# Performance work log

Hardware: AMD Instinct MI355X
Metric: run time of the kernel (lower is better)

The kernel has to match this reference:

```python
import jax, jax.numpy as jnp
import numpy as np

LEAK = 0.01  # torch LeakyReLU default negative_slope

def lrelu(x):
    return jnp.where(x >= 0, x, LEAK * x)

def edge_conv(x, src, dst, ea, W1, b1, W2, b2):
    # message: cat(x_i=target, x_j=source, edge_attr) -> Linear -> LeakyReLU -> Linear
    m = jnp.concatenate([x[dst], x[src], ea], axis=1)          # [E, 2F+Fe]
    h = lrelu(m @ W1 + b1) @ W2 + b2                            # [E, H]
    n = x.shape[0]
    agg = jnp.full((n, h.shape[1]), jnp.inf, h.dtype).at[dst].min(h)  # scatter-min at target
    return jnp.where(jnp.isfinite(agg), agg, jnp.zeros_like(agg))     # empty nodes -> 0


def setup_inputs() -> dict:
    key = jax.random.key(0)
    ks = jax.random.split(key, 20)
    B, N, E = 4, 20000, 640000
    NF, AD, EF, H = 2, 1, 1, 8
    inp = {
        "node_features": jax.random.randint(ks[0], (B, N, NF), 0, 10, dtype=jnp.int32),
        "actions": jax.random.normal(ks[1], (B, N), dtype=jnp.float32),
        "edge_index": jax.random.randint(ks[2], (B, 2, E), 0, N, dtype=jnp.int64),
        "edge_features": jax.random.normal(ks[3], (B, E, EF), dtype=jnp.float32),
    }
    d0 = NF + AD  # 3
    def lin(k, fin, fout):
        s = 1.0 / np.sqrt(fin)
        k1, k2 = jax.random.split(k)
        return (jax.random.uniform(k1, (fin, fout), jnp.float32, -s, s),
                jax.random.uniform(k2, (fout,), jnp.float32, -s, s))
    inp["c1_W1"], inp["c1_b1"] = lin(ks[4], 2 * d0 + EF, H)
    inp["c1_W2"], inp["c1_b2"] = lin(ks[5], H, H)
    inp["c2_W1"], inp["c2_b1"] = lin(ks[6], 2 * H + 1, H)
    inp["c2_W2"], inp["c2_b2"] = lin(ks[7], H, H)
    inp["c3_W1"], inp["c3_b1"] = lin(ks[8], 2 * H + 1, H)
    inp["c3_W2"], inp["c3_b2"] = lin(ks[9], H, H)
    inp["lin_W"], inp["lin_b"] = lin(ks[10], d0 + H, 1)
    return inp


def reference(node_features, actions, edge_index, edge_features,
              c1_W1, c1_b1, c1_W2, c1_b2,
              c2_W1, c2_b1, c2_W2, c2_b2,
              c3_W1, c3_b1, c3_W2, c3_b2,
              lin_W, lin_b):
    # x = int(node_features) concat actions  -> float
    x0 = jnp.concatenate([node_features.astype(jnp.int32).astype(jnp.float32),
                          actions[..., None]], axis=-1)  # [B,N,3]

    def per_graph(x0g, eig, eag):
        src, dst = eig[0], eig[1]  # flow source_to_target: x_j=src, x_i=dst
        h = lrelu(edge_conv(x0g, src, dst, eag, c1_W1, c1_b1, c1_W2, c1_b2))
        h = lrelu(edge_conv(h, src, dst, eag, c2_W1, c2_b1, c2_W2, c2_b2))
        h = lrelu(edge_conv(h, src, dst, eag, c3_W1, c3_b1, c3_W2, c3_b2))
        xc = jnp.concatenate([x0g, h], axis=1)  # [N, 3+8]
        return jnp.sum(xc, axis=0)              # sum-pool over nodes

    pooled = jax.vmap(per_graph)(x0, edge_index, edge_features)  # [B, 11]
    return pooled @ lin_W + lin_b  # [B, 1]
```

## Files before the change

kernel.cpp:

```cpp
#include <hip/hip_runtime.h>

#define LEAK 0.01f
#define BS 128
#define PCHUNK 4096
#define PT 512
#define CT 512
#define MAXNB 256
#define CPGMAX 256

__device__ __forceinline__ float lrelu(float v) {
    return v >= 0.f ? v : LEAK * v;
}

__device__ __forceinline__ unsigned int fmin_encode(float x) {
    unsigned int u = __float_as_uint(x);
    return (u & 0x80000000u) ? ~u : (u | 0x80000000u);
}
__device__ __forceinline__ float fmin_decode(unsigned int k) {
    unsigned int u = (k & 0x80000000u) ? (k ^ 0x80000000u) : ~k;
    return __uint_as_float(u);
}

__device__ __forceinline__ unsigned int bf16_rne(float f) {
    unsigned int u = __float_as_uint(f);
    return (u + 0x7FFFu + ((u >> 16) & 1u)) >> 16;
}

__device__ __forceinline__ void block_add(float c, float* dst) {
    __shared__ float wsum[8];
#pragma unroll
    for (int off = 32; off > 0; off >>= 1) c += __shfl_down(c, off, 64);
    int lane = threadIdx.x & 63;
    int wave = threadIdx.x >> 6;
    if (lane == 0) wsum[wave] = c;
    __syncthreads();
    if (threadIdx.x == 0) {
        float s = 0.f;
        int nw = blockDim.x >> 6;
        for (int w = 0; w < nw; ++w) s += wsum[w];
        atomicAdd(dst, s);
    }
}

__global__ __launch_bounds__(PT) void part_init_kernel(
    const int* __restrict__ ei, const float* __restrict__ ea,
    int2* __restrict__ pairs, int* __restrict__ ofs,
    const int* __restrict__ nf, const float* __restrict__ act,
    const float* __restrict__ W1, const float* __restrict__ b1,
    const float* __restrict__ lw, const float* __restrict__ lb,
    float* __restrict__ a1, unsigned short* __restrict__ a2,
    float* __restrict__ out, int E, int N, int NB, int CPG) {
    int b = blockIdx.y;
    int t = threadIdx.x;

    if (blockIdx.x >= CPG) {
        int n = (blockIdx.x - CPG) * PT + t;
        float c = 0.f;
        if (n < N) {
            size_t i = (size_t)b * N + n;
            float x0 = (float)nf[i * 2 + 0];
            float x1 = (float)nf[i * 2 + 1];
            float x2 = act[i];
            float v1[8], v2[8];
#pragma unroll
            for (int j = 0; j < 8; ++j) {
                v1[j] = b1[j] + x0 * W1[0 * 8 + j] + x1 * W1[1 * 8 + j] + x2 * W1[2 * 8 + j];
                v2[j] =         x0 * W1[3 * 8 + j] + x1 * W1[4 * 8 + j] + x2 * W1[5 * 8 + j];
            }
            float4* o1 = (float4*)(a1 + i * 8);
            o1[0] = make_float4(v1[0], v1[1], v1[2], v1[3]);
            o1[1] = make_float4(v1[4], v1[5], v1[6], v1[7]);
            unsigned int w[4];
#pragma unroll
            for (int q = 0; q < 4; ++q)
                w[q] = bf16_rne(v2[2 * q]) | (bf16_rne(v2[2 * q + 1]) << 16);
            *(int4*)(a2 + i * 8) = make_int4(w[0], w[1], w[2], w[3]);
            c = x0 * lw[0] + x1 * lw[1] + x2 * lw[2];
            if (n == 0) c += lb[0];
        }
        block_add(c, &out[b]);
        return;
    }

    __shared__ int lc[MAXNB];
    __shared__ int lofs[MAXNB + 1];
    __shared__ int ts[PT];
    int c = blockIdx.x;
    for (int i = t; i < NB; i += PT) lc[i] = 0;
    __syncthreads();

    int e0 = c * PCHUNK;
    int end = min(e0 + PCHUNK, E);
    const int* srow = ei + (size_t)b * 2 * E;
    const int* drow = srow + E;

    int pk[PCHUNK / PT];
#pragma unroll
    for (int j = 0; j < PCHUNK / PT; ++j) {
        int e = e0 + j * PT + t;
        int p = -1;
        if (e < end) {
            int d = drow[e];
            int bin = d >> 7;
            int r = atomicAdd(&lc[bin], 1);
            p = bin | ((d & 127) << 10) | (r << 17);
        }
        pk[j] = p;
    }
    __syncthreads();

    int v = (t < NB) ? lc[t] : 0;
    ts[t] = v;
    __syncthreads();
    int incl = v;
    for (int off = 1; off < PT; off <<= 1) {
        int add = (t >= off) ? ts[t - off] : 0;
        __syncthreads();
        incl += add;
        ts[t] = incl;
        __syncthreads();
    }
    if (t < NB) lofs[t] = incl - v;
    if (t == PT - 1) lofs[NB] = incl;
    __syncthreads();

    for (int i = t; i <= NB; i += PT) {
        int w = lofs[i];
        ofs[((size_t)b * (NB + 1) + i) * CPG + c] = w;
        if (i < NB) lc[i] = w;
    }
    __syncthreads();

    size_t pbase = (size_t)b * E + e0;
#pragma unroll
    for (int j = 0; j < PCHUNK / PT; ++j) {
        int e = e0 + j * PT + t;
        if (e < end) {
            int p = pk[j];
            int bin = p & 1023;
            int dl = (p >> 10) & 127;
            int r = p >> 17;
            int pos = lc[bin] + r;
            pairs[pbase + pos] =
                make_int2(srow[e] | (dl << 16), __float_as_int(ea[(size_t)b * E + e]));
        }
    }
}


__device__ __forceinline__ void conv_edge_compute(
    const float* we, const float* bb, const float* __restrict__ W2,
    int2 p, int4 raw, const float* __restrict__ a1s,
    unsigned int* __restrict__ acc) {
    int dl = (p.x >> 16) & 127;
    float eav = __int_as_float(p.y);
    unsigned int wq[4] = {(unsigned int)raw.x, (unsigned int)raw.y,
                          (unsigned int)raw.z, (unsigned int)raw.w};
    float a2v[8];
#pragma unroll
    for (int q = 0; q < 4; ++q) {
        a2v[2 * q]     = __uint_as_float(wq[q] << 16);
        a2v[2 * q + 1] = __uint_as_float(wq[q] & 0xFFFF0000u);
    }
    float h1[8];
#pragma unroll
    for (int j = 0; j < 8; ++j) {
        h1[j] = a1s[dl * 9 + j] + a2v[j];
        h1[j] = fmaf(eav, we[j], h1[j]);
        h1[j] = lrelu(h1[j]);
    }
    float h2[8];
#pragma unroll
    for (int j = 0; j < 8; ++j) h2[j] = bb[j];
#pragma unroll
    for (int kk = 0; kk < 8; ++kk) {
        float hk = h1[kk];
#pragma unroll
        for (int j = 0; j < 8; ++j) h2[j] = fmaf(hk, W2[kk * 8 + j], h2[j]);
    }
#pragma unroll
    for (int j = 0; j < 8; ++j)
        atomicMin(&acc[dl * 9 + j], fmin_encode(h2[j]));
}

__device__ __forceinline__ void conv_edges_runs(
    const unsigned short* __restrict__ a2g, const float* we, const float* bb,
    const float* __restrict__ W2, const int2* __restrict__ pairsg,
    const int* __restrict__ ofb, int CPG,
    const float* __restrict__ a1s, unsigned int* __restrict__ acc,
    int* __restrict__ rs, int* __restrict__ re) {
    int t = threadIdx.x;
    for (int c = t; c < CPG; c += CT) {
        rs[c] = ofb[c];
        re[c] = ofb[CPG + c];
    }
    __syncthreads();
    int sw = t >> 5, sub = t & 31;
    const int nsw = CT >> 5;
    int c = sw;
    int2 pcur = make_int2(0, 0);
    int4 vcur = make_int4(0, 0, 0, 0);
    int kcur = 0, k1cur = 0;
    bool haveCur = false;
    if (c < CPG) {
        int cb = c * PCHUNK;
        kcur = cb + rs[c] + sub;
        k1cur = cb + re[c];
        if (kcur < k1cur) {
            pcur = pairsg[kcur];
            vcur = *(const int4*)(a2g + (size_t)(pcur.x & 0xFFFF) * 8);
            haveCur = true;
        }
    }
    while (c < CPG) {
        int cn = c + nsw;
        int2 pnext = make_int2(0, 0);
        int4 vnext = make_int4(0, 0, 0, 0);
        int knext = 0, k1next = 0;
        bool haveNext = false;
        if (cn < CPG) {
            int cb = cn * PCHUNK;
            knext = cb + rs[cn] + sub;
            k1next = cb + re[cn];
            if (knext < k1next) {
                pnext = pairsg[knext];
                vnext = *(const int4*)(a2g + (size_t)(pnext.x & 0xFFFF) * 8);
                haveNext = true;
            }
        }
        if (haveCur) {
            conv_edge_compute(we, bb, W2, pcur, vcur, a1s, acc);
            for (int k = kcur + 32; k < k1cur; k += 32) {
                int2 p = pairsg[k];
                int4 v = *(const int4*)(a2g + (size_t)(p.x & 0xFFFF) * 8);
                conv_edge_compute(we, bb, W2, p, v, a1s, acc);
            }
        }
        c = cn; pcur = pnext; vcur = vnext; kcur = knext; k1cur = k1next;
        haveCur = haveNext;
    }
}

__global__ __launch_bounds__(CT) void conv_mid_kernel(
    const float* __restrict__ a1, const unsigned short* __restrict__ a2,
    const float* __restrict__ w1e, const float* __restrict__ W2,
    const float* __restrict__ b2,
    const float* __restrict__ nW1, const float* __restrict__ nb1,
    const int* __restrict__ ofs, const int2* __restrict__ pairs,
    float* __restrict__ na1, unsigned short* __restrict__ na2,
    int N, int NB, int CPG, int E) {
    __shared__ float a1s[BS * 9];
    __shared__ unsigned int acc[BS * 9];
    __shared__ int rs[CPGMAX];
    __shared__ int re[CPGMAX];
    int b = blockIdx.y;
    int bin = blockIdx.x;
    int n0 = bin << 7;
    int nCnt = min(BS, N - n0);
    int t = threadIdx.x;
    size_t node0 = (size_t)b * N + n0;

    for (int i = t; i < nCnt * 8; i += CT)
        a1s[(i >> 3) * 9 + (i & 7)] = a1[node0 * 8 + i];
    for (int i = t; i < BS * 9; i += CT) acc[i] = 0xFFFFFFFFu;
    float we[8], bb[8];
#pragma unroll
    for (int j = 0; j < 8; ++j) { we[j] = w1e[j]; bb[j] = b2[j]; }
    __syncthreads();

    conv_edges_runs(a2 + (size_t)b * N * 8, we, bb, W2,
                    pairs + (size_t)b * E,
                    ofs + ((size_t)b * (NB + 1) + bin) * CPG,
                    CPG, a1s, acc, rs, re);
    __syncthreads();

    for (int i = t; i < nCnt * 8; i += CT) {
        float v = fmin_decode(acc[(i >> 3) * 9 + (i & 7)]);
        unsigned int u = __float_as_uint(v);
        if ((u & 0x7F800000u) == 0x7F800000u) v = 0.f;
        a1s[(i >> 3) * 9 + (i & 7)] = lrelu(v);
    }
    __syncthreads();

    for (int nh = t; nh < nCnt * 2; nh += CT) {
        int node = nh >> 1, half = nh & 1;
        float h[8];
#pragma unroll
        for (int j = 0; j < 8; ++j) h[j] = a1s[node * 9 + j];
        float v[8];
#pragma unroll
        for (int j = 0; j < 8; ++j) v[j] = half ? 0.f : nb1[j];
        const float* Wbase = nW1 + (half ? 64 : 0);
#pragma unroll
        for (int k = 0; k < 8; ++k) {
            float hk = h[k];
#pragma unroll
            for (int j = 0; j < 8; ++j) v[j] = fmaf(hk, Wbase[k * 8 + j], v[j]);
        }
        if (half) {
            unsigned int w[4];
#pragma unroll
            for (int q = 0; q < 4; ++q)
                w[q] = bf16_rne(v[2 * q]) | (bf16_rne(v[2 * q + 1]) << 16);
            *(int4*)(na2 + (node0 + node) * 8) = make_int4(w[0], w[1], w[2], w[3]);
        } else {
            float4* o = (float4*)(na1 + (node0 + node) * 8);
            o[0] = make_float4(v[0], v[1], v[2], v[3]);
            o[1] = make_float4(v[4], v[5], v[6], v[7]);
        }
    }
}

__global__ __launch_bounds__(CT) void conv_final_kernel(
    const float* __restrict__ a1, const unsigned short* __restrict__ a2,
    const float* __restrict__ w1e, const float* __restrict__ W2,
    const float* __restrict__ b2, const float* __restrict__ lw,
    const int* __restrict__ ofs, const int2* __restrict__ pairs,
    float* __restrict__ out, int N, int NB, int CPG, int E) {
    __shared__ float a1s[BS * 9];
    __shared__ unsigned int acc[BS * 9];
    __shared__ int rs[CPGMAX];
    __shared__ int re[CPGMAX];
    int b = blockIdx.y;
    int bin = blockIdx.x;
    int n0 = bin << 7;
    int nCnt = min(BS, N - n0);
    int t = threadIdx.x;
    size_t node0 = (size_t)b * N + n0;

    for (int i = t; i < nCnt * 8; i += CT)
        a1s[(i >> 3) * 9 + (i & 7)] = a1[node0 * 8 + i];
    for (int i = t; i < BS * 9; i += CT) acc[i] = 0xFFFFFFFFu;
    float we[8], bb[8];
#pragma unroll
    for (int j = 0; j < 8; ++j) { we[j] = w1e[j]; bb[j] = b2[j]; }
    __syncthreads();

    conv_edges_runs(a2 + (size_t)b * N * 8, we, bb, W2,
                    pairs + (size_t)b * E,
                    ofs + ((size_t)b * (NB + 1) + bin) * CPG,
                    CPG, a1s, acc, rs, re);
    __syncthreads();

    float c = 0.f;
    if (t < nCnt) {
#pragma unroll
        for (int j = 0; j < 8; ++j) {
            float v = fmin_decode(acc[t * 9 + j]);
            unsigned int u = __float_as_uint(v);
            if ((u & 0x7F800000u) == 0x7F800000u) v = 0.f;
            c = fmaf(lrelu(v), lw[3 + j], c);
        }
    }
    __syncthreads();
    block_add(c, &out[b]);
}


__global__ __launch_bounds__(256) void node_init_kernel(
    const int* __restrict__ nf, const float* __restrict__ act,
    float* __restrict__ x0, int BN) {
    int tid = blockIdx.x * blockDim.x + threadIdx.x;
    if (tid >= BN) return;
    x0[tid * 3 + 0] = (float)nf[tid * 2 + 0];
    x0[tid * 3 + 1] = (float)nf[tid * 2 + 1];
    x0[tid * 3 + 2] = act[tid];
}

template <int D>
__global__ __launch_bounds__(256) void edge_conv_kernel(
    const float* __restrict__ x, const int* __restrict__ ei,
    const float* __restrict__ ea,
    const float* __restrict__ W1, const float* __restrict__ b1,
    const float* __restrict__ W2, const float* __restrict__ b2,
    unsigned int* __restrict__ agg, int E, int N, int B) {
    int tid = blockIdx.x * blockDim.x + threadIdx.x;
    if (tid >= B * E) return;
    int b = tid / E;
    int e = tid - b * E;
    const int* eb = ei + (size_t)b * 2 * E;
    int s = eb[e];
    int d = eb[E + e];
    const float* xi = x + ((size_t)b * N + d) * D;
    const float* xj = x + ((size_t)b * N + s) * D;
    constexpr int M = 2 * D + 1;
    float m[M];
#pragma unroll
    for (int k = 0; k < D; ++k) { m[k] = xi[k]; m[D + k] = xj[k]; }
    m[2 * D] = ea[(size_t)b * E + e];
    float h1[8];
#pragma unroll
    for (int j = 0; j < 8; ++j) h1[j] = b1[j];
#pragma unroll
    for (int k = 0; k < M; ++k) {
        float mk = m[k];
#pragma unroll
        for (int j = 0; j < 8; ++j) h1[j] = fmaf(mk, W1[k * 8 + j], h1[j]);
    }
#pragma unroll
    for (int j = 0; j < 8; ++j) h1[j] = lrelu(h1[j]);
    float h2[8];
#pragma unroll
    for (int j = 0; j < 8; ++j) h2[j] = b2[j];
#pragma unroll
    for (int k = 0; k < 8; ++k) {
        float hk = h1[k];
#pragma unroll
        for (int j = 0; j < 8; ++j) h2[j] = fmaf(hk, W2[k * 8 + j], h2[j]);
    }
    unsigned int* ag = agg + ((size_t)b * N + d) * 8;
#pragma unroll
    for (int j = 0; j < 8; ++j) atomicMin(&ag[j], fmin_encode(h2[j]));
}

__global__ __launch_bounds__(256) void finalize_kernel(
    unsigned int* __restrict__ agg, int total) {
    int tid = blockIdx.x * blockDim.x + threadIdx.x;
    if (tid >= total) return;
    float v = fmin_decode(agg[tid]);
    unsigned int u = __float_as_uint(v);
    if ((u & 0x7F800000u) == 0x7F800000u) v = 0.f;
    ((float*)agg)[tid] = lrelu(v);
}

__global__ __launch_bounds__(256) void pool_kernel(
    const float* __restrict__ x0, const float* __restrict__ h,
    const float* __restrict__ lw, const float* __restrict__ lb,
    float* __restrict__ out, int N) {
    int b = blockIdx.y;
    int n = blockIdx.x * blockDim.x + threadIdx.x;
    float c = 0.f;
    if (n < N) {
        const float* x = x0 + ((size_t)b * N + n) * 3;
        const float* hh = h + ((size_t)b * N + n) * 8;
        c = x[0] * lw[0] + x[1] * lw[1] + x[2] * lw[2];
#pragma unroll
        for (int k = 0; k < 8; ++k) c = fmaf(hh[k], lw[3 + k], c);
        if (n == 0) c += lb[0];
    }
    block_add(c, &out[b]);
}


static inline size_t align256(size_t x) { return (x + 255) & ~(size_t)255; }

extern "C" void kernel_launch(void* const* d_in, const int* in_sizes, int n_in,
                              void* d_out, int out_size, void* d_ws, size_t ws_size,
                              hipStream_t stream) {
    const int B = 4;
    const int N = in_sizes[1] / B;
    const int E = in_sizes[2] / (2 * B);

    const int*   nf  = (const int*)d_in[0];
    const float* act = (const float*)d_in[1];
    const int*   ei  = (const int*)d_in[2];
    const float* ea  = (const float*)d_in[3];
    const float* c1_W1 = (const float*)d_in[4];
    const float* c1_b1 = (const float*)d_in[5];
    const float* c1_W2 = (const float*)d_in[6];
    const float* c1_b2 = (const float*)d_in[7];
    const float* c2_W1 = (const float*)d_in[8];
    const float* c2_b1 = (const float*)d_in[9];
    const float* c2_W2 = (const float*)d_in[10];
    const float* c2_b2 = (const float*)d_in[11];
    const float* c3_W1 = (const float*)d_in[12];
    const float* c3_b1 = (const float*)d_in[13];
    const float* c3_W2 = (const float*)d_in[14];
    const float* c3_b2 = (const float*)d_in[15];
    const float* lw    = (const float*)d_in[16];
    const float* lb    = (const float*)d_in[17];
    float* out = (float*)d_out;

    const int BN = B * N;
    const int BE = B * E;
    const int NB = (N + BS - 1) / BS;
    const int CPG = (E + PCHUNK - 1) / PCHUNK;

    char* ws = (char*)d_ws;
    size_t off = 0;
    float* a1A = (float*)(ws + off);           off += align256((size_t)BN * 8 * 4);
    float* a1B = (float*)(ws + off);           off += align256((size_t)BN * 8 * 4);
    unsigned short* a2A = (unsigned short*)(ws + off); off += align256((size_t)BN * 8 * 2);
    unsigned short* a2B = (unsigned short*)(ws + off); off += align256((size_t)BN * 8 * 2);
    int* ofs    = (int*)(ws + off);    off += align256((size_t)B * (NB + 1) * CPG * 4);
    int2* pairs = (int2*)(ws + off);   off += align256((size_t)BE * 8);
    float* x0   = (float*)(ws + off);  off += align256((size_t)BN * 3 * 4);
    const bool useFast = (off <= ws_size) && (NB <= MAXNB) && (CPG <= CPGMAX) &&
                         (N <= 32768);

    hipMemsetAsync(out, 0, (size_t)B * sizeof(float), stream);

    if (useFast) {
        const int initBlocks = (N + PT - 1) / PT;
        dim3 pgrid(CPG + initBlocks, B);
        dim3 cgrid(NB, B);

        part_init_kernel<<<pgrid, PT, 0, stream>>>(
            ei, ea, pairs, ofs, nf, act, c1_W1, c1_b1, lw, lb,
            a1A, a2A, out, E, N, NB, CPG);

        conv_mid_kernel<<<cgrid, CT, 0, stream>>>(
            a1A, a2A, c1_W1 + 6 * 8, c1_W2, c1_b2, c2_W1, c2_b1,
            ofs, pairs, a1B, a2B, N, NB, CPG, E);
        conv_mid_kernel<<<cgrid, CT, 0, stream>>>(
            a1B, a2B, c2_W1 + 16 * 8, c2_W2, c2_b2, c3_W1, c3_b1,
            ofs, pairs, a1A, a2A, N, NB, CPG, E);
        conv_final_kernel<<<cgrid, CT, 0, stream>>>(
            a1A, a2A, c3_W1 + 16 * 8, c3_W2, c3_b2, lw,
            ofs, pairs, out, N, NB, CPG, E);
    } else {
        const int egrid = (BE + 255) / 256;
        const int aggTotal = BN * 8;
        const int agrid = (aggTotal + 255) / 256;
        const size_t aggBytes = (size_t)aggTotal * 4;
        unsigned int* uA = (unsigned int*)a1A;
        unsigned int* uB = (unsigned int*)a1B;

        node_init_kernel<<<(BN + 255) / 256, 256, 0, stream>>>(nf, act, x0, BN);

        hipMemsetAsync(uA, 0xFF, aggBytes, stream);
        edge_conv_kernel<3><<<egrid, 256, 0, stream>>>(
            x0, ei, ea, c1_W1, c1_b1, c1_W2, c1_b2, uA, E, N, B);
        finalize_kernel<<<agrid, 256, 0, stream>>>(uA, aggTotal);

        hipMemsetAsync(uB, 0xFF, aggBytes, stream);
        edge_conv_kernel<8><<<egrid, 256, 0, stream>>>(
            (const float*)uA, ei, ea, c2_W1, c2_b1, c2_W2, c2_b2, uB, E, N, B);
        finalize_kernel<<<agrid, 256, 0, stream>>>(uB, aggTotal);

        hipMemsetAsync(uA, 0xFF, aggBytes, stream);
        edge_conv_kernel<8><<<egrid, 256, 0, stream>>>(
            (const float*)uB, ei, ea, c3_W1, c3_b1, c3_W2, c3_b2, uA, E, N, B);
        finalize_kernel<<<agrid, 256, 0, stream>>>(uA, aggTotal);

        dim3 plgrid((N + 255) / 256, B);
        pool_kernel<<<plgrid, 256, 0, stream>>>(x0, (const float*)uA, lw, lb, out, N);
    }
}
```

Measured before the change: 219.7 us.

## Fuse partition and three conv stages into one cooperative kernel with grid syncs

Merges the partition/init kernel and the three edge-conv stage kernels into a single cooperative mega-kernel that separates stages with grid.sync and threadfence. This removes three kernel launch boundaries and the associated drain and refill gaps. The launch is used only when occupancy allows the whole grid (max(CPG+initBlocks, NB) × B blocks) to be resident, and falls back to the separate kernels otherwise. It also drops the software prefetch of the next chunk in the edge loop, and the mega-kernel carries the union of shared memory with launch bounds of 8 blocks, which may change register allocation.

Result: faster. 208.7 us (median of 2 runs) (-5.0%).

```diff
diff --git a/kernel.cpp b/kernel.cpp
--- a/kernel.cpp
+++ b/kernel.cpp
@@ -1,4 +1,7 @@
 #include <hip/hip_runtime.h>
+#include <hip/hip_cooperative_groups.h>
+
+namespace cg = cooperative_groups;
 
 #define LEAK 0.01f
 #define BS 128
@@ -42,50 +45,47 @@
     }
 }
 
-__global__ __launch_bounds__(PT) void part_init_kernel(
-    const int* __restrict__ ei, const float* __restrict__ ea,
-    int2* __restrict__ pairs, int* __restrict__ ofs,
+
+__device__ void init_body(
     const int* __restrict__ nf, const float* __restrict__ act,
     const float* __restrict__ W1, const float* __restrict__ b1,
     const float* __restrict__ lw, const float* __restrict__ lb,
     float* __restrict__ a1, unsigned short* __restrict__ a2,
-    float* __restrict__ out, int E, int N, int NB, int CPG) {
-    int b = blockIdx.y;
+    float* __restrict__ out, int N, int b, int ib) {
     int t = threadIdx.x;
-
-    if (blockIdx.x >= CPG) {
-        int n = (blockIdx.x - CPG) * PT + t;
-        float c = 0.f;
-        if (n < N) {
-            size_t i = (size_t)b * N + n;
-            float x0 = (float)nf[i * 2 + 0];
-            float x1 = (float)nf[i * 2 + 1];
-            float x2 = act[i];
-            float v1[8], v2[8];
-#pragma unroll
-            for (int j = 0; j < 8; ++j) {
-                v1[j] = b1[j] + x0 * W1[0 * 8 + j] + x1 * W1[1 * 8 + j] + x2 * W1[2 * 8 + j];
-                v2[j] =         x0 * W1[3 * 8 + j] + x1 * W1[4 * 8 + j] + x2 * W1[5 * 8 + j];
-            }
-            float4* o1 = (float4*)(a1 + i * 8);
-            o1[0] = make_float4(v1[0], v1[1], v1[2], v1[3]);
-            o1[1] = make_float4(v1[4], v1[5], v1[6], v1[7]);
-            unsigned int w[4];
-#pragma unroll
-            for (int q = 0; q < 4; ++q)
-                w[q] = bf16_rne(v2[2 * q]) | (bf16_rne(v2[2 * q + 1]) << 16);
-            *(int4*)(a2 + i * 8) = make_int4(w[0], w[1], w[2], w[3]);
-            c = x0 * lw[0] + x1 * lw[1] + x2 * lw[2];
-            if (n == 0) c += lb[0];
-        }
-        block_add(c, &out[b]);
-        return;
-    }
-
-    __shared__ int lc[MAXNB];
-    __shared__ int lofs[MAXNB + 1];
-    __shared__ int ts[PT];
-    int c = blockIdx.x;
+    int n = ib * PT + t;
+    float c = 0.f;
+    if (n < N) {
+        size_t i = (size_t)b * N + n;
+        float x0 = (float)nf[i * 2 + 0];
+        float x1 = (float)nf[i * 2 + 1];
+        float x2 = act[i];
+        float v1[8], v2[8];
+#pragma unroll
+        for (int j = 0; j < 8; ++j) {
+            v1[j] = b1[j] + x0 * W1[0 * 8 + j] + x1 * W1[1 * 8 + j] + x2 * W1[2 * 8 + j];
+            v2[j] =         x0 * W1[3 * 8 + j] + x1 * W1[4 * 8 + j] + x2 * W1[5 * 8 + j];
+        }
+        float4* o1 = (float4*)(a1 + i * 8);
+        o1[0] = make_float4(v1[0], v1[1], v1[2], v1[3]);
+        o1[1] = make_float4(v1[4], v1[5], v1[6], v1[7]);
+        unsigned int w[4];
+#pragma unroll
+        for (int q = 0; q < 4; ++q)
+            w[q] = bf16_rne(v2[2 * q]) | (bf16_rne(v2[2 * q + 1]) << 16);
+        *(int4*)(a2 + i * 8) = make_int4(w[0], w[1], w[2], w[3]);
+        c = x0 * lw[0] + x1 * lw[1] + x2 * lw[2];
+        if (n == 0) c += lb[0];
+    }
+    block_add(c, &out[b]);
+}
+
+__device__ void part_body(
+    const int* __restrict__ ei, const float* __restrict__ ea,
+    int2* __restrict__ pairs, int* __restrict__ ofs,
+    int E, int NB, int CPG, int b, int c,
+    int* __restrict__ lc, int* __restrict__ lofs, int* __restrict__ ts) {
+    int t = threadIdx.x;
     for (int i = t; i < NB; i += PT) lc[i] = 0;
     __syncthreads();
 
@@ -147,7 +147,6 @@
     }
 }
 
-
 __device__ __forceinline__ void conv_edge_compute(
     const float* we, const float* bb, const float* __restrict__ W2,
     int2 p, int4 raw, const float* __restrict__ a1s,
@@ -183,7 +182,7 @@
         atomicMin(&acc[dl * 9 + j], fmin_encode(h2[j]));
 }
 
-__device__ __forceinline__ void conv_edges_runs(
+__device__ void conv_edges_runs(
     const unsigned short* __restrict__ a2g, const float* we, const float* bb,
     const float* __restrict__ W2, const int2* __restrict__ pairsg,
     const int* __restrict__ ofb, int CPG,
@@ -197,48 +196,193 @@
     __syncthreads();
     int sw = t >> 5, sub = t & 31;
     const int nsw = CT >> 5;
-    int c = sw;
-    int2 pcur = make_int2(0, 0);
-    int4 vcur = make_int4(0, 0, 0, 0);
-    int kcur = 0, k1cur = 0;
-    bool haveCur = false;
-    if (c < CPG) {
+    for (int c = sw; c < CPG; c += nsw) {
         int cb = c * PCHUNK;
-        kcur = cb + rs[c] + sub;
-        k1cur = cb + re[c];
-        if (kcur < k1cur) {
-            pcur = pairsg[kcur];
-            vcur = *(const int4*)(a2g + (size_t)(pcur.x & 0xFFFF) * 8);
-            haveCur = true;
-        }
-    }
-    while (c < CPG) {
-        int cn = c + nsw;
-        int2 pnext = make_int2(0, 0);
-        int4 vnext = make_int4(0, 0, 0, 0);
-        int knext = 0, k1next = 0;
-        bool haveNext = false;
-        if (cn < CPG) {
-            int cb = cn * PCHUNK;
-            knext = cb + rs[cn] + sub;
-            k1next = cb + re[cn];
-            if (knext < k1next) {
-                pnext = pairsg[knext];
-                vnext = *(const int4*)(a2g + (size_t)(pnext.x & 0xFFFF) * 8);
-                haveNext = true;
-            }
-        }
-        if (haveCur) {
-            conv_edge_compute(we, bb, W2, pcur, vcur, a1s, acc);
-            for (int k = kcur + 32; k < k1cur; k += 32) {
-                int2 p = pairsg[k];
-                int4 v = *(const int4*)(a2g + (size_t)(p.x & 0xFFFF) * 8);
-                conv_edge_compute(we, bb, W2, p, v, a1s, acc);
-            }
-        }
-        c = cn; pcur = pnext; vcur = vnext; kcur = knext; k1cur = k1next;
-        haveCur = haveNext;
-    }
+        int k1 = cb + re[c];
+        for (int k = cb + rs[c] + sub; k < k1; k += 32) {
+            int2 p = pairsg[k];
+            int4 v = *(const int4*)(a2g + (size_t)(p.x & 0xFFFF) * 8);
+            conv_edge_compute(we, bb, W2, p, v, a1s, acc);
+        }
+    }
+}
+
+__device__ void conv_mid_body(
+    const float* __restrict__ a1, const unsigned short* __restrict__ a2,
+    const float* __restrict__ w1e, const float* __restrict__ W2,
+    const float* __restrict__ b2,
+    const float* __restrict__ nW1, const float* __restrict__ nb1,
+    const int* __restrict__ ofs, const int2* __restrict__ pairs,
+    float* __restrict__ na1, unsigned short* __restrict__ na2,
+    int N, int NB, int CPG, int E, int b, int bin,
+    float* __restrict__ a1s, unsigned int* __restrict__ acc,
+    int* __restrict__ rs, int* __restrict__ re) {
+    int n0 = bin << 7;
+    int nCnt = min(BS, N - n0);
+    int t = threadIdx.x;
+    size_t node0 = (size_t)b * N + n0;
+
+    for (int i = t; i < nCnt * 8; i += CT)
+        a1s[(i >> 3) * 9 + (i & 7)] = a1[node0 * 8 + i];
+    for (int i = t; i < BS * 9; i += CT) acc[i] = 0xFFFFFFFFu;
+    float we[8], bb[8];
+#pragma unroll
+    for (int j = 0; j < 8; ++j) { we[j] = w1e[j]; bb[j] = b2[j]; }
+    __syncthreads();
+
+    conv_edges_runs(a2 + (size_t)b * N * 8, we, bb, W2,
+                    pairs + (size_t)b * E,
+                    ofs + ((size_t)b * (NB + 1) + bin) * CPG,
+                    CPG, a1s, acc, rs, re);
+    __syncthreads();
+
+    for (int i = t; i < nCnt * 8; i += CT) {
+        float v = fmin_decode(acc[(i >> 3) * 9 + (i & 7)]);
+        unsigned int u = __float_as_uint(v);
+        if ((u & 0x7F800000u) == 0x7F800000u) v = 0.f;
+        a1s[(i >> 3) * 9 + (i & 7)] = lrelu(v);
+    }
+    __syncthreads();
+
+    for (int nh = t; nh < nCnt * 2; nh += CT) {
+        int node = nh >> 1, half = nh & 1;
+        float h[8];
+#pragma unroll
+        for (int j = 0; j < 8; ++j) h[j] = a1s[node * 9 + j];
+        float v[8];
+#pragma unroll
+        for (int j = 0; j < 8; ++j) v[j] = half ? 0.f : nb1[j];
+        const float* Wbase = nW1 + (half ? 64 : 0);
+#pragma unroll
+        for (int k = 0; k < 8; ++k) {
+            float hk = h[k];
+#pragma unroll
+            for (int j = 0; j < 8; ++j) v[j] = fmaf(hk, Wbase[k * 8 + j], v[j]);
+        }
+        if (half) {
+            unsigned int w[4];
+#pragma unroll
+            for (int q = 0; q < 4; ++q)
+                w[q] = bf16_rne(v[2 * q]) | (bf16_rne(v[2 * q + 1]) << 16);
+            *(int4*)(na2 + (node0 + node) * 8) = make_int4(w[0], w[1], w[2], w[3]);
+        } else {
+            float4* o = (float4*)(na1 + (node0 + node) * 8);
+            o[0] = make_float4(v[0], v[1], v[2], v[3]);
+            o[1] = make_float4(v[4], v[5], v[6], v[7]);
+        }
+    }
+    __syncthreads();
+}
+
+__device__ void conv_final_body(
+    const float* __restrict__ a1, const unsigned short* __restrict__ a2,
+    const float* __restrict__ w1e, const float* __restrict__ W2,
+    const float* __restrict__ b2, const float* __restrict__ lw,
+    const int* __restrict__ ofs, const int2* __restrict__ pairs,
+    float* __restrict__ out, int N, int NB, int CPG, int E, int b, int bin,
+    float* __restrict__ a1s, unsigned int* __restrict__ acc,
+    int* __restrict__ rs, int* __restrict__ re) {
+    int n0 = bin << 7;
+    int nCnt = min(BS, N - n0);
+    int t = threadIdx.x;
+    size_t node0 = (size_t)b * N + n0;
+
+    for (int i = t; i < nCnt * 8; i += CT)
+        a1s[(i >> 3) * 9 + (i & 7)] = a1[node0 * 8 + i];
+    for (int i = t; i < BS * 9; i += CT) acc[i] = 0xFFFFFFFFu;
+    float we[8], bb[8];
+#pragma unroll
+    for (int j = 0; j < 8; ++j) { we[j] = w1e[j]; bb[j] = b2[j]; }
+    __syncthreads();
+
+    conv_edges_runs(a2 + (size_t)b * N * 8, we, bb, W2,
+                    pairs + (size_t)b * E,
+                    ofs + ((size_t)b * (NB + 1) + bin) * CPG,
+                    CPG, a1s, acc, rs, re);
+    __syncthreads();
+
+    float c = 0.f;
+    if (t < nCnt) {
+#pragma unroll
+        for (int j = 0; j < 8; ++j) {
+            float v = fmin_decode(acc[t * 9 + j]);
+            unsigned int u = __float_as_uint(v);
+            if ((u & 0x7F800000u) == 0x7F800000u) v = 0.f;
+            c = fmaf(lrelu(v), lw[3 + j], c);
+        }
+    }
+    __syncthreads();
+    block_add(c, &out[b]);
+}
+
+
+struct MegaParams {
+    const int* ei; const float* ea;
+    int2* pairs; int* ofs;
+    const int* nf; const float* act;
+    const float* W11; const float* b11; const float* W21; const float* b21;
+    const float* W12; const float* b12; const float* W22; const float* b22;
+    const float* W13; const float* b13; const float* W23; const float* b23;
+    const float* lw; const float* lb;
+    float* a1A; unsigned short* a2A; float* a1B; unsigned short* a2B;
+    float* out;
+    int E, N, NB, CPG, initBlocks;
+};
+
+__global__ __launch_bounds__(512, 8) void mega_kernel(MegaParams P) {
+    cg::grid_group grid = cg::this_grid();
+    __shared__ int lc[MAXNB];
+    __shared__ int lofs[MAXNB + 1];
+    __shared__ int ts[PT];
+    __shared__ float a1s[BS * 9];
+    __shared__ unsigned int acc[BS * 9];
+    __shared__ int rs[CPGMAX];
+    __shared__ int re[CPGMAX];
+    int b = blockIdx.y, bx = blockIdx.x;
+
+    if (bx < P.CPG)
+        part_body(P.ei, P.ea, P.pairs, P.ofs, P.E, P.NB, P.CPG, b, bx, lc, lofs, ts);
+    else if (bx - P.CPG < P.initBlocks)
+        init_body(P.nf, P.act, P.W11, P.b11, P.lw, P.lb, P.a1A, P.a2A, P.out,
+                  P.N, b, bx - P.CPG);
+    __threadfence();
+    grid.sync();
+    if (bx < P.NB)
+        conv_mid_body(P.a1A, P.a2A, P.W11 + 6 * 8, P.W21, P.b21, P.W12, P.b12,
+                      P.ofs, P.pairs, P.a1B, P.a2B, P.N, P.NB, P.CPG, P.E,
+                      b, bx, a1s, acc, rs, re);
+    __threadfence();
+    grid.sync();
+    if (bx < P.NB)
+        conv_mid_body(P.a1B, P.a2B, P.W12 + 16 * 8, P.W22, P.b22, P.W13, P.b13,
+                      P.ofs, P.pairs, P.a1A, P.a2A, P.N, P.NB, P.CPG, P.E,
+                      b, bx, a1s, acc, rs, re);
+    __threadfence();
+    grid.sync();
+    if (bx < P.NB)
+        conv_final_body(P.a1A, P.a2A, P.W13 + 16 * 8, P.W23, P.b23, P.lw,
+                        P.ofs, P.pairs, P.out, P.N, P.NB, P.CPG, P.E,
+                        b, bx, a1s, acc, rs, re);
+}
+
+
+__global__ __launch_bounds__(PT) void part_init_kernel(
+    const int* __restrict__ ei, const float* __restrict__ ea,
+    int2* __restrict__ pairs, int* __restrict__ ofs,
+    const int* __restrict__ nf, const float* __restrict__ act,
+    const float* __restrict__ W1, const float* __restrict__ b1,
+    const float* __restrict__ lw, const float* __restrict__ lb,
+    float* __restrict__ a1, unsigned short* __restrict__ a2,
+    float* __restrict__ out, int E, int N, int NB, int CPG) {
+    __shared__ int lc[MAXNB];
+    __shared__ int lofs[MAXNB + 1];
+    __shared__ int ts[PT];
+    int b = blockIdx.y;
+    if (blockIdx.x >= CPG) {
+        init_body(nf, act, W1, b1, lw, lb, a1, a2, out, N, b, blockIdx.x - CPG);
+        return;
+    }
+    part_body(ei, ea, pairs, ofs, E, NB, CPG, b, blockIdx.x, lc, lofs, ts);
 }
 
 __global__ __launch_bounds__(CT) void conv_mid_kernel(
@@ -253,62 +397,8 @@
     __shared__ unsigned int acc[BS * 9];
     __shared__ int rs[CPGMAX];
     __shared__ int re[CPGMAX];
-    int b = blockIdx.y;
-    int bin = blockIdx.x;
-    int n0 = bin << 7;
-    int nCnt = min(BS, N - n0);
-    int t = threadIdx.x;
-    size_t node0 = (size_t)b * N + n0;
-
-    for (int i = t; i < nCnt * 8; i += CT)
-        a1s[(i >> 3) * 9 + (i & 7)] = a1[node0 * 8 + i];
-    for (int i = t; i < BS * 9; i += CT) acc[i] = 0xFFFFFFFFu;
-    float we[8], bb[8];
-#pragma unroll
-    for (int j = 0; j < 8; ++j) { we[j] = w1e[j]; bb[j] = b2[j]; }
-    __syncthreads();
-
-    conv_edges_runs(a2 + (size_t)b * N * 8, we, bb, W2,
-                    pairs + (size_t)b * E,
-                    ofs + ((size_t)b * (NB + 1) + bin) * CPG,
-                    CPG, a1s, acc, rs, re);
-    __syncthreads();
-
-    for (int i = t; i < nCnt * 8; i += CT) {
-        float v = fmin_decode(acc[(i >> 3) * 9 + (i & 7)]);
-        unsigned int u = __float_as_uint(v);
-        if ((u & 0x7F800000u) == 0x7F800000u) v = 0.f;
-        a1s[(i >> 3) * 9 + (i & 7)] = lrelu(v);
-    }
-    __syncthreads();
-
-    for (int nh = t; nh < nCnt * 2; nh += CT) {
-        int node = nh >> 1, half = nh & 1;
-        float h[8];
-#pragma unroll
-        for (int j = 0; j < 8; ++j) h[j] = a1s[node * 9 + j];
-        float v[8];
-#pragma unroll
-        for (int j = 0; j < 8; ++j) v[j] = half ? 0.f : nb1[j];
-        const float* Wbase = nW1 + (half ? 64 : 0);
-#pragma unroll
-        for (int k = 0; k < 8; ++k) {
-            float hk = h[k];
-#pragma unroll
-            for (int j = 0; j < 8; ++j) v[j] = fmaf(hk, Wbase[k * 8 + j], v[j]);
-        }
-        if (half) {
-            unsigned int w[4];
-#pragma unroll
-            for (int q = 0; q < 4; ++q)
-                w[q] = bf16_rne(v[2 * q]) | (bf16_rne(v[2 * q + 1]) << 16);
-            *(int4*)(na2 + (node0 + node) * 8) = make_int4(w[0], w[1], w[2], w[3]);
-        } else {
-            float4* o = (float4*)(na1 + (node0 + node) * 8);
-            o[0] = make_float4(v[0], v[1], v[2], v[3]);
-            o[1] = make_float4(v[4], v[5], v[6], v[7]);
-        }
-    }
+    conv_mid_body(a1, a2, w1e, W2, b2, nW1, nb1, ofs, pairs, na1, na2,
+                  N, NB, CPG, E, blockIdx.y, blockIdx.x, a1s, acc, rs, re);
 }
 
 __global__ __launch_bounds__(CT) void conv_final_kernel(
@@ -321,39 +411,8 @@
     __shared__ unsigned int acc[BS * 9];
     __shared__ int rs[CPGMAX];
     __shared__ int re[CPGMAX];
-    int b = blockIdx.y;
-    int bin = blockIdx.x;
-    int n0 = bin << 7;
-    int nCnt = min(BS, N - n0);
-    int t = threadIdx.x;
-    size_t node0 = (size_t)b * N + n0;
-
-    for (int i = t; i < nCnt * 8; i += CT)
-        a1s[(i >> 3) * 9 + (i & 7)] = a1[node0 * 8 + i];
-    for (int i = t; i < BS * 9; i += CT) acc[i] = 0xFFFFFFFFu;
-    float we[8], bb[8];
-#pragma unroll
-    for (int j = 0; j < 8; ++j) { we[j] = w1e[j]; bb[j] = b2[j]; }
-    __syncthreads();
-
-    conv_edges_runs(a2 + (size_t)b * N * 8, we, bb, W2,
-                    pairs + (size_t)b * E,
-                    ofs + ((size_t)b * (NB + 1) + bin) * CPG,
-                    CPG, a1s, acc, rs, re);
-    __syncthreads();
-
-    float c = 0.f;
-    if (t < nCnt) {
-#pragma unroll
-        for (int j = 0; j < 8; ++j) {
-            float v = fmin_decode(acc[t * 9 + j]);
-            unsigned int u = __float_as_uint(v);
-            if ((u & 0x7F800000u) == 0x7F800000u) v = 0.f;
-            c = fmaf(lrelu(v), lw[3 + j], c);
-        }
-    }
-    __syncthreads();
-    block_add(c, &out[b]);
+    conv_final_body(a1, a2, w1e, W2, b2, lw, ofs, pairs, out,
+                    N, NB, CPG, E, blockIdx.y, blockIdx.x, a1s, acc, rs, re);
 }
 
 
@@ -475,6 +534,7 @@
     const int BE = B * E;
     const int NB = (N + BS - 1) / BS;
     const int CPG = (E + PCHUNK - 1) / PCHUNK;
+    const int initBlocks = (N + PT - 1) / PT;
 
     char* ws = (char*)d_ws;
     size_t off = 0;
@@ -491,23 +551,47 @@
     hipMemsetAsync(out, 0, (size_t)B * sizeof(float), stream);
 
     if (useFast) {
-        const int initBlocks = (N + PT - 1) / PT;
-        dim3 pgrid(CPG + initBlocks, B);
-        dim3 cgrid(NB, B);
-
-        part_init_kernel<<<pgrid, PT, 0, stream>>>(
-            ei, ea, pairs, ofs, nf, act, c1_W1, c1_b1, lw, lb,
-            a1A, a2A, out, E, N, NB, CPG);
-
-        conv_mid_kernel<<<cgrid, CT, 0, stream>>>(
-            a1A, a2A, c1_W1 + 6 * 8, c1_W2, c1_b2, c2_W1, c2_b1,
-            ofs, pairs, a1B, a2B, N, NB, CPG, E);
-        conv_mid_kernel<<<cgrid, CT, 0, stream>>>(
-            a1B, a2B, c2_W1 + 16 * 8, c2_W2, c2_b2, c3_W1, c3_b1,
-            ofs, pairs, a1A, a2A, N, NB, CPG, E);
-        conv_final_kernel<<<cgrid, CT, 0, stream>>>(
-            a1A, a2A, c3_W1 + 16 * 8, c3_W2, c3_b2, lw,
-            ofs, pairs, out, N, NB, CPG, E);
+        const int gx = (CPG + initBlocks > NB) ? (CPG + initBlocks) : NB;
+
+        int dev = 0;
+        hipGetDevice(&dev);
+        int numCU = 0;
+        hipDeviceGetAttribute(&numCU, hipDeviceAttributeMultiprocessorCount, dev);
+        int occ = 0;
+        hipOccupancyMaxActiveBlocksPerMultiprocessor(&occ, mega_kernel, 512, 0);
+        const bool canCoop = (occ > 0) && ((size_t)occ * (size_t)numCU >=
+                                           (size_t)gx * (size_t)B);
+
+        if (canCoop) {
+            MegaParams P;
+            P.ei = ei; P.ea = ea; P.pairs = pairs; P.ofs = ofs;
+            P.nf = nf; P.act = act;
+            P.W11 = c1_W1; P.b11 = c1_b1; P.W21 = c1_W2; P.b21 = c1_b2;
+            P.W12 = c2_W1; P.b12 = c2_b1; P.W22 = c2_W2; P.b22 = c2_b2;
+            P.W13 = c3_W1; P.b13 = c3_b1; P.W23 = c3_W2; P.b23 = c3_b2;
+            P.lw = lw; P.lb = lb;
+            P.a1A = a1A; P.a2A = a2A; P.a1B = a1B; P.a2B = a2B;
+            P.out = out;
+            P.E = E; P.N = N; P.NB = NB; P.CPG = CPG; P.initBlocks = initBlocks;
+            void* args[] = {&P};
+            hipLaunchCooperativeKernel((void*)mega_kernel, dim3(gx, B),
+                                       dim3(512), args, 0, stream);
+        } else {
+            dim3 pgrid(CPG + initBlocks, B);
+            dim3 cgrid(NB, B);
+            part_init_kernel<<<pgrid, PT, 0, stream>>>(
+                ei, ea, pairs, ofs, nf, act, c1_W1, c1_b1, lw, lb,
+                a1A, a2A, out, E, N, NB, CPG);
+            conv_mid_kernel<<<cgrid, CT, 0, stream>>>(
+                a1A, a2A, c1_W1 + 6 * 8, c1_W2, c1_b2, c2_W1, c2_b1,
+                ofs, pairs, a1B, a2B, N, NB, CPG, E);
+            conv_mid_kernel<<<cgrid, CT, 0, stream>>>(
+                a1B, a2B, c2_W1 + 16 * 8, c2_W2, c2_b2, c3_W1, c3_b1,
+                ofs, pairs, a1A, a2A, N, NB, CPG, E);
+            conv_final_kernel<<<cgrid, CT, 0, stream>>>(
+                a1A, a2A, c3_W1 + 16 * 8, c3_W2, c3_b2, lw,
+                ofs, pairs, out, N, NB, CPG, E);
+        }
     } else {
         const int egrid = (BE + 255) / 256;
         const int aggTotal = BN * 8;
```
